# Optimization experiments

Hardware: AMD Instinct MI355X
Metric: run time of the kernel (lower is better)

## Reference

```python
import jax, jax.numpy as jnp
import numpy as np

B, L, H, NB, D, DH = 8, 4096, 16, 8, 1024, 128

def setup_inputs() -> dict:
    key = jax.random.key(0)
    ks = jax.random.split(key, 12)
    theta_path = jax.random.normal(ks[0], (B, L, H, NB), jnp.float32)
    content_emb = jax.random.normal(ks[1], (B, L, D), jnp.float32)
    s_in = 1.0 / np.sqrt(D).astype(np.float32)
    s_h = 1.0 / np.sqrt(DH).astype(np.float32)
    # log_R_head: Linear(D,128) -> GELU -> Linear(128, H*NB), last layer weight *0.01, bias 0
    r_w1 = jax.random.normal(ks[2], (D, DH), jnp.float32) * s_in
    r_b1 = jnp.zeros((DH,), jnp.float32)
    r_w2 = jax.random.normal(ks[3], (DH, H * NB), jnp.float32) * s_h * 0.01
    r_b2 = jnp.zeros((H * NB,), jnp.float32)
    # measure_head
    m_w1 = jax.random.normal(ks[4], (D, DH), jnp.float32) * s_in
    m_b1 = jax.random.normal(ks[5], (DH,), jnp.float32) * s_in
    m_w2 = jax.random.normal(ks[6], (DH, H * NB), jnp.float32) * s_h
    m_b2 = jax.random.normal(ks[7], (H * NB,), jnp.float32) * s_h
    log_Q = jnp.full((H, NB), -3.0, jnp.float32)
    log_R_avg = jnp.full((H, NB), 1.0, jnp.float32)
    return {"theta_path": theta_path, "content_emb": content_emb,
            "log_Q": log_Q, "log_R_avg": log_R_avg,
            "r_w1": r_w1, "r_b1": r_b1, "r_w2": r_w2, "r_b2": r_b2,
            "m_w1": m_w1, "m_b1": m_b1, "m_w2": m_w2, "m_b2": m_b2}

def _mlp(x, w1, b1, w2, b2):
    h = jax.nn.gelu(x @ w1 + b1, approximate=False)  # torch nn.GELU default = exact
    return h @ w2 + b2

def reference(theta_path, content_emb, log_Q, log_R_avg,
              r_w1, r_b1, r_w2, r_b2, m_w1, m_b1, m_w2, m_b2):
    b, l, h, nb = theta_path.shape
    log_R = jnp.clip(_mlp(content_emb, r_w1, r_b1, r_w2, r_b2).reshape(b, l, h, nb), -5.0, 5.0)
    R = jnp.exp(log_R)
    z = jnp.pi * jnp.tanh(_mlp(content_emb, m_w1, m_b1, m_w2, m_b2).reshape(b, l, h, nb))
    diff = z - theta_path
    nu = jnp.arctan2(jnp.sin(diff), jnp.cos(diff))  # wrap angle error to (-pi, pi]
    Q = jnp.exp(log_Q)
    Ravg = jnp.exp(log_R_avg)
    Pi_dare = 0.5 * (-Q + jnp.sqrt(Q * Q + 4.0 * Q * Ravg))  # [H, NB]
    Pi = jnp.broadcast_to(Pi_dare[None, None], (b, l, h, nb))
    K = Pi / jnp.maximum(Pi + R, 1e-8)
    alpha = 1.0 - K
    u = K * nu
    # affine associative scan over sequence dim: d_t = alpha_t * d_{t-1} + u_t
    def combine(c1, c2):
        a1, u1 = c1
        a2, u2 = c2
        return (a2 * a1, a2 * u1 + u2)
    _, d = jax.lax.associative_scan(combine, (alpha, u), axis=1)
    return (theta_path + d, Pi, K, R)
```

## Files before the change

### kernel.cpp

```cpp
#include <hip/hip_runtime.h>
#include <hip/hip_bf16.h>
#include <cstdint>
#include <cstddef>

#define TOK 32768
#define CCH 128
#define DIN 1024

typedef __attribute__((ext_vector_type(8))) short short8;
typedef __attribute__((ext_vector_type(4))) float f32x4;

#define LIST_CAP 262144u

static __device__ __forceinline__ uint16_t f2bf(float f) {
  __hip_bfloat16 h = __float2bfloat16(f);
  return __builtin_bit_cast(uint16_t, h);
}
static __device__ __forceinline__ float bf2f(uint16_t u) {
  __hip_bfloat16 h = __builtin_bit_cast(__hip_bfloat16, u);
  return __bfloat162float(h);
}
static __device__ __forceinline__ void splitbf(float x, uint16_t& hi, uint16_t& lo) {
  hi = f2bf(x);
  lo = f2bf(x - bf2f(hi));
}

__global__ void prep_kernel(const float* __restrict__ r_w1, const float* __restrict__ r_w2,
                            const float* __restrict__ m_w1, const float* __restrict__ m_w2,
                            const float* __restrict__ logQ, const float* __restrict__ logRavg,
                            uint16_t* __restrict__ W1r, uint16_t* __restrict__ W2r,
                            uint16_t* __restrict__ W1mh, uint16_t* __restrict__ W1ml,
                            uint16_t* __restrict__ W2mh, uint16_t* __restrict__ W2ml,
                            float* __restrict__ PiArr, unsigned int* __restrict__ cnt)
{
  int idx = blockIdx.x * 256 + threadIdx.x;
  if (idx == 0) cnt[0] = 0;
  if (idx < 131072) {
    int e = idx;
    int j = e & 7, lane = (e >> 3) & 63, nt = (e >> 9) & 7, c = (e >> 12) & 1, kt = e >> 13;
    int k = kt * 64 + c * 32 + (lane >> 4) * 8 + j;
    int n = nt * 16 + (lane & 15);
    W1r[e] = f2bf(r_w1[k * 128 + n]);
  } else if (idx < 147456) {
    int e = idx - 131072;
    int j = e & 7, l = (e >> 3) & 63, c = (e >> 9) & 3, t = e >> 11;
    int k = c * 32 + (l >> 4) * 8 + j;
    int col = t * 16 + (l & 15);
    W2r[e] = f2bf(r_w2[k * 128 + col]);
  } else if (idx < 278528) {
    int e = idx - 147456;
    int j = e & 7, lane = (e >> 3) & 63, nt = (e >> 9) & 7, c = (e >> 12) & 1, kt = e >> 13;
    int k = kt * 64 + c * 32 + (lane >> 4) * 8 + j;
    int n = nt * 16 + (lane & 15);
    uint16_t h, l;
    splitbf(m_w1[k * 128 + n], h, l);
    W1mh[e] = h; W1ml[e] = l;
  } else if (idx < 294912) {
    int e = idx - 278528;
    int j = e & 7, l = (e >> 3) & 63, c = (e >> 9) & 3, t = e >> 11;
    int k = c * 32 + (l >> 4) * 8 + j;
    int col = t * 16 + (l & 15);
    uint16_t h, lo;
    splitbf(m_w2[k * 128 + col], h, lo);
    W2mh[e] = h; W2ml[e] = lo;
  } else if (idx < 295040) {
    int i = idx - 294912;
    float Q = expf(logQ[i]);
    float Rv = expf(logRavg[i]);
    PiArr[i] = 0.5f * (-Q + sqrtf(Q * Q + 4.0f * Q * Rv));
  }
}

__global__ __launch_bounds__(512, 4) void fused_all(
    const float* __restrict__ X, const float* __restrict__ theta,
    const uint16_t* __restrict__ W1r, const uint16_t* __restrict__ W2r,
    const uint16_t* __restrict__ W1h, const uint16_t* __restrict__ W1l,
    const uint16_t* __restrict__ W2h, const uint16_t* __restrict__ W2l,
    const float* __restrict__ rB1, const float* __restrict__ rB2,
    const float* __restrict__ B1, const float* __restrict__ B2,
    const float* __restrict__ PiArr,
    float* __restrict__ out0, float* __restrict__ out1,
    float* __restrict__ out2, float* __restrict__ out3,
    float* __restrict__ AggA, float* __restrict__ AggU,
    unsigned int* __restrict__ cnt, unsigned int* __restrict__ list)
{
  union SM {
    struct { uint16_t Xh[2][64][64]; uint16_t Xl[2][64][64]; } s1;
    struct { uint16_t Hh[64][128]; uint16_t Hl[64][128]; uint16_t Hr[64][128]; } s2;
    struct { float2 Agg[4][4][128]; } s3;
  };
  __shared__ SM sm;

  const int tid = threadIdx.x;
  const int w = tid >> 6, lane = tid & 63;
  const int l15 = lane & 15, l4 = lane >> 4;
  const int tn = w;
  const int tok0 = blockIdx.x * 64;

  f32x4 accm[4], accr[4];
#pragma unroll
  for (int m = 0; m < 4; ++m) { accm[m] = 0.0f; accr[m] = 0.0f; }

  const int rr = tid >> 4, cc = tid & 15;
  const int wofs = (cc * 8) ^ ((rr & 7) << 4);
  float4 xa0, xa1;

  auto ldX = [&](int kt, float4& v0, float4& v1) {
    v0 = *reinterpret_cast<const float4*>(
        X + (size_t)(tok0 + rr) * DIN + kt * 64 + cc * 4);
    v1 = *reinterpret_cast<const float4*>(
        X + (size_t)(tok0 + rr + 32) * DIN + kt * 64 + cc * 4);
  };
  auto wrX = [&](int b, const float4& v0, const float4& v1) {
    ushort4 vh, vl;
    splitbf(v0.x, vh.x, vl.x);
    splitbf(v0.y, vh.y, vl.y);
    splitbf(v0.z, vh.z, vl.z);
    splitbf(v0.w, vh.w, vl.w);
    *reinterpret_cast<ushort4*>((char*)&sm.s1.Xh[b][rr][0] + wofs) = vh;
    *reinterpret_cast<ushort4*>((char*)&sm.s1.Xl[b][rr][0] + wofs) = vl;
    splitbf(v1.x, vh.x, vl.x);
    splitbf(v1.y, vh.y, vl.y);
    splitbf(v1.z, vh.z, vl.z);
    splitbf(v1.w, vh.w, vl.w);
    *reinterpret_cast<ushort4*>((char*)&sm.s1.Xh[b][rr + 32][0] + wofs) = vh;
    *reinterpret_cast<ushort4*>((char*)&sm.s1.Xl[b][rr + 32][0] + wofs) = vl;
  };
  auto ldB = [&](int kt, short8 (&h)[2], short8 (&l)[2], short8 (&r)[2]) {
#pragma unroll
    for (int c = 0; c < 2; ++c) {
      const size_t boff = (size_t)((((kt * 2 + c) * 8 + tn) * 64 + lane) * 8);
      h[c] = *reinterpret_cast<const short8*>(W1h + boff);
      l[c] = *reinterpret_cast<const short8*>(W1l + boff);
      r[c] = *reinterpret_cast<const short8*>(W1r + boff);
    }
  };

  short8 bhc[2], blc[2], brc[2], bhn[2], bln[2], brn[2];
  ldX(0, xa0, xa1);
  wrX(0, xa0, xa1);
  ldB(0, bhc, blc, brc);
  __syncthreads();

#pragma unroll
  for (int kt = 0; kt < 16; ++kt) {
    const int cur = kt & 1;

    if (kt < 15) {
      ldX(kt + 1, xa0, xa1);
      ldB(kt + 1, bhn, bln, brn);
    }

#pragma unroll
    for (int c = 0; c < 2; ++c) {
#pragma unroll
      for (int m = 0; m < 4; ++m) {
        const int row = m * 16 + l15;
        const int ob = (c * 64 + l4 * 16) ^ ((l15 & 7) << 4);
        const short8 ah = *reinterpret_cast<const short8*>((const char*)&sm.s1.Xh[cur][row][0] + ob);
        const short8 al = *reinterpret_cast<const short8*>((const char*)&sm.s1.Xl[cur][row][0] + ob);
        accm[m] = __builtin_amdgcn_mfma_f32_16x16x32_bf16(ah, bhc[c], accm[m], 0, 0, 0);
        accm[m] = __builtin_amdgcn_mfma_f32_16x16x32_bf16(al, bhc[c], accm[m], 0, 0, 0);
        accm[m] = __builtin_amdgcn_mfma_f32_16x16x32_bf16(ah, blc[c], accm[m], 0, 0, 0);
        accr[m] = __builtin_amdgcn_mfma_f32_16x16x32_bf16(ah, brc[c], accr[m], 0, 0, 0);
      }
    }

    if (kt < 15) wrX(cur ^ 1, xa0, xa1);
    __syncthreads();

#pragma unroll
    for (int c = 0; c < 2; ++c) { bhc[c] = bhn[c]; blc[c] = bln[c]; brc[c] = brn[c]; }
  }

  short8 b2h[4], b2l[4], b2r[4];
#pragma unroll
  for (int c2 = 0; c2 < 4; ++c2) {
    const size_t boff = (size_t)(((tn * 4 + c2) * 64 + lane) * 8);
    b2h[c2] = *reinterpret_cast<const short8*>(W2h + boff);
    b2l[c2] = *reinterpret_cast<const short8*>(W2l + boff);
    b2r[c2] = *reinterpret_cast<const short8*>(W2r + boff);
  }

  const int n = tn * 16 + l15;
  {
    const float b1m = B1[n];
    const float b1rr = rB1[n];
#pragma unroll
    for (int m = 0; m < 4; ++m)
#pragma unroll
      for (int r = 0; r < 4; ++r) {
        const int row = m * 16 + l4 * 4 + r;
        const int ob = (2 * n) ^ ((row & 7) << 4);
        const float v = accm[m][r] + b1m;
        const float ev = erff(v / 1.41421356237309515f);
        const float g = 0.5f * v * (ev + 1.0f);
        uint16_t gh, gl;
        splitbf(g, gh, gl);
        *reinterpret_cast<uint16_t*>((char*)&sm.s2.Hh[row][0] + ob) = gh;
        *reinterpret_cast<uint16_t*>((char*)&sm.s2.Hl[row][0] + ob) = gl;
        const float vr = accr[m][r] + b1rr;
        const float gr = 0.5f * vr * (1.0f + erff(vr * 0.70710678118654752f));
        *reinterpret_cast<uint16_t*>((char*)&sm.s2.Hr[row][0] + ob) = f2bf(gr);
      }
  }
  __syncthreads();

  f32x4 acc2m[4], acc2r[4];
#pragma unroll
  for (int m = 0; m < 4; ++m) { acc2m[m] = 0.0f; acc2r[m] = 0.0f; }

#pragma unroll
  for (int c2 = 0; c2 < 4; ++c2) {
#pragma unroll
    for (int m = 0; m < 4; ++m) {
      const int row = m * 16 + l15;
      const int ob = (c2 * 64 + l4 * 16) ^ ((l15 & 7) << 4);
      const short8 ah = *reinterpret_cast<const short8*>((const char*)&sm.s2.Hh[row][0] + ob);
      const short8 al = *reinterpret_cast<const short8*>((const char*)&sm.s2.Hl[row][0] + ob);
      const short8 ar = *reinterpret_cast<const short8*>((const char*)&sm.s2.Hr[row][0] + ob);
      acc2m[m] = __builtin_amdgcn_mfma_f32_16x16x32_bf16(ah, b2h[c2], acc2m[m], 0, 0, 0);
      acc2m[m] = __builtin_amdgcn_mfma_f32_16x16x32_bf16(al, b2h[c2], acc2m[m], 0, 0, 0);
      acc2m[m] = __builtin_amdgcn_mfma_f32_16x16x32_bf16(ah, b2l[c2], acc2m[m], 0, 0, 0);
      acc2r[m] = __builtin_amdgcn_mfma_f32_16x16x32_bf16(ar, b2r[c2], acc2r[m], 0, 0, 0);
    }
  }

  {
    const float b2 = rB2[n];
    const float piv = PiArr[n];
#pragma unroll
    for (int m = 0; m < 4; ++m)
#pragma unroll
      for (int r = 0; r < 4; ++r) {
        const int token = tok0 + m * 16 + l4 * 4 + r;
        float lr = acc2r[m][r] + b2;
        lr = fminf(fmaxf(lr, -5.0f), 5.0f);
        const float R = expf(lr);
        const float K = piv / fmaxf(piv + R, 1e-8f);
        const size_t off = (size_t)token * CCH + n;
        out1[off] = piv;
        out2[off] = K;
        out3[off] = R;
        acc2r[m][r] = K;
      }
  }

  {
    const float b2 = B2[n];
#pragma unroll
    for (int m = 0; m < 4; ++m)
#pragma unroll
      for (int r = 0; r < 4; ++r) {
        const int token = tok0 + m * 16 + l4 * 4 + r;
        const float mz = acc2m[m][r] + b2;
        const float z = 3.14159265358979323846f * tanhf(mz);
        const float d = z - theta[(size_t)token * CCH + n];
        const float wr = d - 6.2831853071795864769f * rintf(d * 0.15915494309189533577f);
        if (3.14159265358979323846f - fabsf(wr) < 3e-4f) {
          unsigned int p = atomicAdd(cnt, 1u);
          if (p < LIST_CAP) list[p] = (unsigned int)(token * CCH + n);
        }
        out0[(size_t)token * CCH + n] = wr;
        acc2m[m][r] = wr;
      }
  }

  __syncthreads();
#pragma unroll
  for (int m = 0; m < 4; ++m) {
    float A = 1.0f, U = 0.0f;
#pragma unroll
    for (int r = 0; r < 4; ++r) {
      const float k = acc2r[m][r];
      const float v = acc2m[m][r];
      const float a = 1.0f - k;
      A *= a;
      U = fmaf(a, U, k * v);
    }
    sm.s3.Agg[m][l4][n] = make_float2(A, U);
  }
  __syncthreads();
  if (tid < 128) {
    const int ch = tid;
    float A = 1.0f, U = 0.0f;
#pragma unroll
    for (int g = 0; g < 16; ++g) {
      const float2 au = sm.s3.Agg[g >> 2][g & 3][ch];
      U = fmaf(au.x, U, au.y);
      A *= au.x;
    }
    AggA[blockIdx.x * CCH + ch] = A;
    AggU[blockIdx.x * CCH + ch] = U;
  }
}

__global__ __launch_bounds__(128) void refine_nu(
    const float* __restrict__ X, const float* __restrict__ theta,
    const float* __restrict__ W1, const float* __restrict__ B1,
    const float* __restrict__ W2, const float* __restrict__ B2,
    const unsigned int* __restrict__ cnt, const unsigned int* __restrict__ list,
    float* __restrict__ out0)
{
  __shared__ float h[128];
  const int j = threadIdx.x;
  const unsigned int n = min(cnt[0], LIST_CAP);
  for (unsigned int e = blockIdx.x; e < n; e += gridDim.x) {
    const unsigned int idx = list[e];
    const int tok = (int)(idx >> 7), ch = (int)(idx & 127);
    const float* xr = X + (size_t)tok * DIN;
    float acc = 0.0f;
    for (int k = 0; k < DIN; ++k)
      acc = fmaf(xr[k], W1[(size_t)k * CCH + j], acc);
    const float v = acc + B1[j];
    const float ev = erff(v / 1.41421356237309515f);
    h[j] = 0.5f * v * (ev + 1.0f);
    __syncthreads();
    if (j == 0) {
      float a2 = 0.0f;
      for (int k = 0; k < CCH; ++k)
        a2 = fmaf(h[k], W2[(size_t)k * CCH + ch], a2);
      const float mz = a2 + B2[ch];
      const float z = 3.14159265358979323846f * tanhf(mz);
      const float d = z - theta[(size_t)tok * CCH + ch];
      out0[(size_t)tok * CCH + ch] = atan2f(sinf(d), cosf(d));
    }
    __syncthreads();
  }
}

__global__ __launch_bounds__(64) void refine_agg(
    const float* __restrict__ Kk, const float* __restrict__ nu,
    const unsigned int* __restrict__ cnt, const unsigned int* __restrict__ list,
    float* __restrict__ AggA, float* __restrict__ AggU)
{
  __shared__ float av[64], uv[64];
  const int i = threadIdx.x;
  const unsigned int n = min(cnt[0], LIST_CAP);
  for (unsigned int e = blockIdx.x; e < n; e += gridDim.x) {
    const unsigned int idx = list[e];
    const int ch = (int)(idx & 127);
    const int blk = (int)(idx >> 13);
    const size_t off = (size_t)(blk * 64 + i) * CCH + ch;
    const float k = Kk[off];
    const float v = nu[off];
    av[i] = 1.0f - k;
    uv[i] = k * v;
    __syncthreads();
    if (i == 0) {
      float A = 1.0f, U = 0.0f;
      for (int g = 0; g < 64; ++g) {
        U = fmaf(av[g], U, uv[g]);
        A *= av[g];
      }
      AggA[blk * CCH + ch] = A;
      AggU[blk * CCH + ch] = U;
    }
    __syncthreads();
  }
}

__global__ __launch_bounds__(256) void scan_pass2(
    const float* __restrict__ AggA, const float* __restrict__ AggU,
    float* __restrict__ Carry)
{
  const int wid = blockIdx.x * 4 + (threadIdx.x >> 6);
  const int b = wid >> 7, ch = wid & 127;
  const int g = threadIdx.x & 63;
  const size_t idx = (size_t)(b * 64 + g) * CCH + ch;
  float A = AggA[idx];
  float U = AggU[idx];
#pragma unroll
  for (int s = 1; s < 64; s <<= 1) {
    const float pA = __shfl_up(A, s);
    const float pU = __shfl_up(U, s);
    if (g >= s) {
      U = fmaf(A, pU, U);
      A = A * pA;
    }
  }
  float cU = __shfl_up(U, 1);
  if (g == 0) cU = 0.0f;
  Carry[idx] = cU;
}

__global__ __launch_bounds__(128) void scan_pass3(
    const float* __restrict__ Kk, const float* __restrict__ theta,
    const float* __restrict__ Carry, float* __restrict__ out0)
{
  __shared__ float kb[64 * CCH];
  __shared__ float vb[64 * CCH];
  const int c = threadIdx.x;
  const int blk = blockIdx.x;
  const size_t base = (size_t)blk * 64 * CCH;
#pragma unroll
  for (int i = 0; i < 16; ++i) {
    const int e = i * 128 + c;
    reinterpret_cast<float4*>(kb)[e] = reinterpret_cast<const float4*>(Kk + base)[e];
    reinterpret_cast<float4*>(vb)[e] = reinterpret_cast<const float4*>(out0 + base)[e];
  }
  __syncthreads();
  float d = Carry[blk * CCH + c];
#pragma unroll 8
  for (int i = 0; i < 64; ++i) {
    const float k = kb[i * CCH + c];
    const float v = vb[i * CCH + c];
    d = fmaf(1.0f - k, d, k * v);
    const size_t off = base + (size_t)i * CCH + c;
    out0[off] = theta[off] + d;
  }
}

extern "C" void kernel_launch(void* const* d_in, const int* in_sizes, int n_in,
                              void* d_out, int out_size, void* d_ws, size_t ws_size,
                              hipStream_t stream) {
  const float* theta   = (const float*)d_in[0];
  const float* X       = (const float*)d_in[1];
  const float* logQ    = (const float*)d_in[2];
  const float* logRavg = (const float*)d_in[3];
  const float* r_w1    = (const float*)d_in[4];
  const float* r_b1    = (const float*)d_in[5];
  const float* r_w2    = (const float*)d_in[6];
  const float* r_b2    = (const float*)d_in[7];
  const float* m_w1    = (const float*)d_in[8];
  const float* m_b1    = (const float*)d_in[9];
  const float* m_w2    = (const float*)d_in[10];
  const float* m_b2    = (const float*)d_in[11];

  float* out0 = (float*)d_out;
  float* out1 = out0 + 4194304;
  float* out2 = out0 + 2 * 4194304;
  float* out3 = out0 + 3 * 4194304;

  char* ws = (char*)d_ws;
  uint16_t* W1r  = (uint16_t*)(ws);
  uint16_t* W2r  = (uint16_t*)(ws + 262144);
  float* PiArr   = (float*)(ws + 295936);
  float* AggA    = (float*)(ws + 296448);
  float* AggU    = (float*)(ws + 558592);
  float* Carry   = (float*)(ws + 820736);
  unsigned int* cnt  = (unsigned int*)(ws + 1082880);
  unsigned int* list = (unsigned int*)(ws + 1083136);
  uint16_t* W1mh = (uint16_t*)(ws + 2131712);
  uint16_t* W1ml = (uint16_t*)(ws + 2393856);
  uint16_t* W2mh = (uint16_t*)(ws + 2656000);
  uint16_t* W2ml = (uint16_t*)(ws + 2688768);

  prep_kernel<<<1153, 256, 0, stream>>>(r_w1, r_w2, m_w1, m_w2, logQ, logRavg,
                                        W1r, W2r, W1mh, W1ml, W2mh, W2ml,
                                        PiArr, cnt);
  fused_all<<<512, 512, 0, stream>>>(X, theta, W1r, W2r, W1mh, W1ml, W2mh, W2ml,
                                     r_b1, r_b2, m_b1, m_b2, PiArr,
                                     out0, out1, out2, out3, AggA, AggU, cnt, list);
  refine_nu<<<1024, 128, 0, stream>>>(X, theta, m_w1, m_b1, m_w2, m_b2,
                                      cnt, list, out0);
  refine_agg<<<1024, 64, 0, stream>>>(out2, out0, cnt, list, AggA, AggU);
  scan_pass2<<<256, 256, 0, stream>>>(AggA, AggU, Carry);
  scan_pass3<<<512, 128, 0, stream>>>(out2, theta, Carry, out0);
}
```

Baseline: 123.4 us.

## Process two K-tiles per barrier with a four-stage X shared buffer

The first GEMM loop over the 1024-wide input is restructured to handle two 64-wide K tiles per iteration, with four X buffers in shared memory. That halves the number of __syncthreads barriers and issues two global X loads ahead per iteration. In exchange it uses more registers for the extra prefetched tiles, and the enlarged stage-1 union member raises LDS per block. The W1 fragment load for the second tile is now issued inside the same iteration that consumes it, so that load is less hidden.

```diff
diff --git a/kernel.cpp b/kernel.cpp
--- a/kernel.cpp
+++ b/kernel.cpp
@@ -85,7 +85,7 @@
     unsigned int* __restrict__ cnt, unsigned int* __restrict__ list)
 {
   union SM {
-    struct { uint16_t Xh[2][64][64]; uint16_t Xl[2][64][64]; } s1;
+    struct { uint16_t Xh[4][64][64]; uint16_t Xl[4][64][64]; } s1;
     struct { uint16_t Hh[64][128]; uint16_t Hl[64][128]; uint16_t Hr[64][128]; } s2;
     struct { float2 Agg[4][4][128]; } s3;
   };
@@ -103,7 +103,7 @@
 
   const int rr = tid >> 4, cc = tid & 15;
   const int wofs = (cc * 8) ^ ((rr & 7) << 4);
-  float4 xa0, xa1;
+  float4 xa0, xa1, xb0, xb1;
 
   auto ldX = [&](int kt, float4& v0, float4& v1) {
     v0 = *reinterpret_cast<const float4*>(
@@ -135,42 +135,49 @@
       r[c] = *reinterpret_cast<const short8*>(W1r + boff);
     }
   };
-
-  short8 bhc[2], blc[2], brc[2], bhn[2], bln[2], brn[2];
-  ldX(0, xa0, xa1);
-  wrX(0, xa0, xa1);
-  ldB(0, bhc, blc, brc);
-  __syncthreads();
-
-#pragma unroll
-  for (int kt = 0; kt < 16; ++kt) {
-    const int cur = kt & 1;
-
-    if (kt < 15) {
-      ldX(kt + 1, xa0, xa1);
-      ldB(kt + 1, bhn, bln, brn);
-    }
-
+  auto cluster = [&](int buf, short8 (&bh)[2], short8 (&bl)[2], short8 (&br)[2]) {
 #pragma unroll
     for (int c = 0; c < 2; ++c) {
 #pragma unroll
       for (int m = 0; m < 4; ++m) {
         const int row = m * 16 + l15;
         const int ob = (c * 64 + l4 * 16) ^ ((l15 & 7) << 4);
-        const short8 ah = *reinterpret_cast<const short8*>((const char*)&sm.s1.Xh[cur][row][0] + ob);
-        const short8 al = *reinterpret_cast<const short8*>((const char*)&sm.s1.Xl[cur][row][0] + ob);
-        accm[m] = __builtin_amdgcn_mfma_f32_16x16x32_bf16(ah, bhc[c], accm[m], 0, 0, 0);
-        accm[m] = __builtin_amdgcn_mfma_f32_16x16x32_bf16(al, bhc[c], accm[m], 0, 0, 0);
-        accm[m] = __builtin_amdgcn_mfma_f32_16x16x32_bf16(ah, blc[c], accm[m], 0, 0, 0);
-        accr[m] = __builtin_amdgcn_mfma_f32_16x16x32_bf16(ah, brc[c], accr[m], 0, 0, 0);
+        const short8 ah = *reinterpret_cast<const short8*>((const char*)&sm.s1.Xh[buf][row][0] + ob);
+        const short8 al = *reinterpret_cast<const short8*>((const char*)&sm.s1.Xl[buf][row][0] + ob);
+        accm[m] = __builtin_amdgcn_mfma_f32_16x16x32_bf16(ah, bh[c], accm[m], 0, 0, 0);
+        accm[m] = __builtin_amdgcn_mfma_f32_16x16x32_bf16(al, bh[c], accm[m], 0, 0, 0);
+        accm[m] = __builtin_amdgcn_mfma_f32_16x16x32_bf16(ah, bl[c], accm[m], 0, 0, 0);
+        accr[m] = __builtin_amdgcn_mfma_f32_16x16x32_bf16(ah, br[c], accr[m], 0, 0, 0);
       }
     }
-
-    if (kt < 15) wrX(cur ^ 1, xa0, xa1);
+  };
+
+  short8 bch[2], bcl[2], bcr[2], bnh[2], bnl[2], bnr[2];
+  ldX(0, xa0, xa1);
+  wrX(0, xa0, xa1);
+  ldX(1, xa0, xa1);
+  wrX(1, xa0, xa1);
+  ldB(0, bch, bcl, bcr);
+  __syncthreads();
+
+#pragma unroll
+  for (int i = 0; i < 8; ++i) {
+    const int kt0 = 2 * i, kt1 = 2 * i + 1;
+    if (i < 7) {
+      ldX(kt0 + 2, xa0, xa1);
+      ldX(kt1 + 2, xb0, xb1);
+    }
+    ldB(kt1, bnh, bnl, bnr);
+
+    cluster(kt0 & 3, bch, bcl, bcr);
+    cluster(kt1 & 3, bnh, bnl, bnr);
+
+    if (i < 7) {
+      wrX((kt0 + 2) & 3, xa0, xa1);
+      wrX((kt1 + 2) & 3, xb0, xb1);
+      ldB(kt0 + 2, bch, bcl, bcr);
+    }
     __syncthreads();
-
-#pragma unroll
-    for (int c = 0; c < 2; ++c) { bhc[c] = bhn[c]; blc[c] = bln[c]; brc[c] = brn[c]; }
   }
 
   short8 b2h[4], b2l[4], b2r[4];
```

Result: slower. 131.1 us (+6.3%).

## Retile fused MLP kernel to 2x2 warp grid with split-phase weight prefetch

Applied to the files above, without the earlier changes.

Each of the 8 waves now computes a 32-token by 32-channel tile in a 2x2 (tm,tn) arrangement instead of 64 tokens by 16 channels. Every B-fragment register load and every shared-memory A fragment now feeds two MFMAs, which cuts per-wave LDS reads of the X and H tiles. The first-layer weight prefetch is split into half-step chunks, loaded between the two MFMA clusters, and second-layer weights are double-buffered per k-chunk, which lowers peak register use. The cost is more global weight loads per wave and a changed register and scheduling profile.

```diff
diff --git a/kernel.cpp b/kernel.cpp
--- a/kernel.cpp
+++ b/kernel.cpp
@@ -94,12 +94,14 @@
   const int tid = threadIdx.x;
   const int w = tid >> 6, lane = tid & 63;
   const int l15 = lane & 15, l4 = lane >> 4;
-  const int tn = w;
+  const int tm = w >> 2, tn = w & 3;
   const int tok0 = blockIdx.x * 64;
 
-  f32x4 accm[4], accr[4];
-#pragma unroll
-  for (int m = 0; m < 4; ++m) { accm[m] = 0.0f; accr[m] = 0.0f; }
+  f32x4 accm[2][2], accr[2][2];
+#pragma unroll
+  for (int mm = 0; mm < 2; ++mm)
+#pragma unroll
+    for (int t = 0; t < 2; ++t) { accm[mm][t] = 0.0f; accr[mm][t] = 0.0f; }
 
   const int rr = tid >> 4, cc = tid & 15;
   const int wofs = (cc * 8) ^ ((rr & 7) << 4);
@@ -126,115 +128,129 @@
     *reinterpret_cast<ushort4*>((char*)&sm.s1.Xh[b][rr + 32][0] + wofs) = vh;
     *reinterpret_cast<ushort4*>((char*)&sm.s1.Xl[b][rr + 32][0] + wofs) = vl;
   };
-  auto ldB = [&](int kt, short8 (&h)[2], short8 (&l)[2], short8 (&r)[2]) {
-#pragma unroll
-    for (int c = 0; c < 2; ++c) {
-      const size_t boff = (size_t)((((kt * 2 + c) * 8 + tn) * 64 + lane) * 8);
-      h[c] = *reinterpret_cast<const short8*>(W1h + boff);
-      l[c] = *reinterpret_cast<const short8*>(W1l + boff);
-      r[c] = *reinterpret_cast<const short8*>(W1r + boff);
+  auto ldB = [&](int kt, int c, short8 (&h)[2], short8 (&l)[2], short8 (&r)[2]) {
+#pragma unroll
+    for (int t = 0; t < 2; ++t) {
+      const size_t boff = (size_t)((((kt * 2 + c) * 8 + (tn * 2 + t)) * 64 + lane) * 8);
+      h[t] = *reinterpret_cast<const short8*>(W1h + boff);
+      l[t] = *reinterpret_cast<const short8*>(W1l + boff);
+      r[t] = *reinterpret_cast<const short8*>(W1r + boff);
     }
   };
-
-  short8 bhc[2], blc[2], brc[2], bhn[2], bln[2], brn[2];
+  auto cluster = [&](int buf, int c, short8 (&bh)[2], short8 (&bl)[2], short8 (&br)[2]) {
+#pragma unroll
+    for (int mm = 0; mm < 2; ++mm) {
+      const int row = (tm * 2 + mm) * 16 + l15;
+      const int ob = (c * 64 + l4 * 16) ^ ((l15 & 7) << 4);
+      const short8 ah = *reinterpret_cast<const short8*>((const char*)&sm.s1.Xh[buf][row][0] + ob);
+      const short8 al = *reinterpret_cast<const short8*>((const char*)&sm.s1.Xl[buf][row][0] + ob);
+#pragma unroll
+      for (int t = 0; t < 2; ++t) {
+        accm[mm][t] = __builtin_amdgcn_mfma_f32_16x16x32_bf16(ah, bh[t], accm[mm][t], 0, 0, 0);
+        accm[mm][t] = __builtin_amdgcn_mfma_f32_16x16x32_bf16(al, bh[t], accm[mm][t], 0, 0, 0);
+        accm[mm][t] = __builtin_amdgcn_mfma_f32_16x16x32_bf16(ah, bl[t], accm[mm][t], 0, 0, 0);
+        accr[mm][t] = __builtin_amdgcn_mfma_f32_16x16x32_bf16(ah, br[t], accr[mm][t], 0, 0, 0);
+      }
+    }
+  };
+
+  short8 b0h[2], b0l[2], b0r[2], b1h[2], b1l[2], b1r[2];
   ldX(0, xa0, xa1);
   wrX(0, xa0, xa1);
-  ldB(0, bhc, blc, brc);
+  ldB(0, 0, b0h, b0l, b0r);
   __syncthreads();
 
 #pragma unroll
   for (int kt = 0; kt < 16; ++kt) {
     const int cur = kt & 1;
-
-    if (kt < 15) {
-      ldX(kt + 1, xa0, xa1);
-      ldB(kt + 1, bhn, bln, brn);
-    }
-
-#pragma unroll
-    for (int c = 0; c < 2; ++c) {
-#pragma unroll
-      for (int m = 0; m < 4; ++m) {
-        const int row = m * 16 + l15;
-        const int ob = (c * 64 + l4 * 16) ^ ((l15 & 7) << 4);
-        const short8 ah = *reinterpret_cast<const short8*>((const char*)&sm.s1.Xh[cur][row][0] + ob);
-        const short8 al = *reinterpret_cast<const short8*>((const char*)&sm.s1.Xl[cur][row][0] + ob);
-        accm[m] = __builtin_amdgcn_mfma_f32_16x16x32_bf16(ah, bhc[c], accm[m], 0, 0, 0);
-        accm[m] = __builtin_amdgcn_mfma_f32_16x16x32_bf16(al, bhc[c], accm[m], 0, 0, 0);
-        accm[m] = __builtin_amdgcn_mfma_f32_16x16x32_bf16(ah, blc[c], accm[m], 0, 0, 0);
-        accr[m] = __builtin_amdgcn_mfma_f32_16x16x32_bf16(ah, brc[c], accr[m], 0, 0, 0);
-      }
-    }
-
+    if (kt < 15) ldX(kt + 1, xa0, xa1);
+    ldB(kt, 1, b1h, b1l, b1r);
+    cluster(cur, 0, b0h, b0l, b0r);
+    if (kt < 15) ldB(kt + 1, 0, b0h, b0l, b0r);
+    cluster(cur, 1, b1h, b1l, b1r);
     if (kt < 15) wrX(cur ^ 1, xa0, xa1);
     __syncthreads();
-
-#pragma unroll
-    for (int c = 0; c < 2; ++c) { bhc[c] = bhn[c]; blc[c] = bln[c]; brc[c] = brn[c]; }
-  }
-
-  short8 b2h[4], b2l[4], b2r[4];
-#pragma unroll
-  for (int c2 = 0; c2 < 4; ++c2) {
-    const size_t boff = (size_t)(((tn * 4 + c2) * 64 + lane) * 8);
-    b2h[c2] = *reinterpret_cast<const short8*>(W2h + boff);
-    b2l[c2] = *reinterpret_cast<const short8*>(W2l + boff);
-    b2r[c2] = *reinterpret_cast<const short8*>(W2r + boff);
-  }
-
-  const int n = tn * 16 + l15;
-  {
+  }
+
+#pragma unroll
+  for (int t = 0; t < 2; ++t) {
+    const int n = (tn * 2 + t) * 16 + l15;
     const float b1m = B1[n];
     const float b1rr = rB1[n];
 #pragma unroll
-    for (int m = 0; m < 4; ++m)
+    for (int mm = 0; mm < 2; ++mm)
 #pragma unroll
       for (int r = 0; r < 4; ++r) {
-        const int row = m * 16 + l4 * 4 + r;
+        const int row = (tm * 2 + mm) * 16 + l4 * 4 + r;
         const int ob = (2 * n) ^ ((row & 7) << 4);
-        const float v = accm[m][r] + b1m;
+        const float v = accm[mm][t][r] + b1m;
         const float ev = erff(v / 1.41421356237309515f);
         const float g = 0.5f * v * (ev + 1.0f);
         uint16_t gh, gl;
         splitbf(g, gh, gl);
         *reinterpret_cast<uint16_t*>((char*)&sm.s2.Hh[row][0] + ob) = gh;
         *reinterpret_cast<uint16_t*>((char*)&sm.s2.Hl[row][0] + ob) = gl;
-        const float vr = accr[m][r] + b1rr;
+        const float vr = accr[mm][t][r] + b1rr;
         const float gr = 0.5f * vr * (1.0f + erff(vr * 0.70710678118654752f));
         *reinterpret_cast<uint16_t*>((char*)&sm.s2.Hr[row][0] + ob) = f2bf(gr);
       }
   }
   __syncthreads();
 
-  f32x4 acc2m[4], acc2r[4];
-#pragma unroll
-  for (int m = 0; m < 4; ++m) { acc2m[m] = 0.0f; acc2r[m] = 0.0f; }
-
+  f32x4 acc2m[2][2], acc2r[2][2];
+#pragma unroll
+  for (int mm = 0; mm < 2; ++mm)
+#pragma unroll
+    for (int t = 0; t < 2; ++t) { acc2m[mm][t] = 0.0f; acc2r[mm][t] = 0.0f; }
+
+  short8 w2h[2][2], w2l[2][2], w2r[2][2];
+#pragma unroll
+  for (int t = 0; t < 2; ++t) {
+    const size_t boff = (size_t)((((tn * 2 + t) * 4 + 0) * 64 + lane) * 8);
+    w2h[0][t] = *reinterpret_cast<const short8*>(W2h + boff);
+    w2l[0][t] = *reinterpret_cast<const short8*>(W2l + boff);
+    w2r[0][t] = *reinterpret_cast<const short8*>(W2r + boff);
+  }
 #pragma unroll
   for (int c2 = 0; c2 < 4; ++c2) {
-#pragma unroll
-    for (int m = 0; m < 4; ++m) {
-      const int row = m * 16 + l15;
+    const int cb = c2 & 1;
+    if (c2 < 3) {
+#pragma unroll
+      for (int t = 0; t < 2; ++t) {
+        const size_t boff = (size_t)((((tn * 2 + t) * 4 + (c2 + 1)) * 64 + lane) * 8);
+        w2h[cb ^ 1][t] = *reinterpret_cast<const short8*>(W2h + boff);
+        w2l[cb ^ 1][t] = *reinterpret_cast<const short8*>(W2l + boff);
+        w2r[cb ^ 1][t] = *reinterpret_cast<const short8*>(W2r + boff);
+      }
+    }
+#pragma unroll
+    for (int mm = 0; mm < 2; ++mm) {
+      const int row = (tm * 2 + mm) * 16 + l15;
       const int ob = (c2 * 64 + l4 * 16) ^ ((l15 & 7) << 4);
       const short8 ah = *reinterpret_cast<const short8*>((const char*)&sm.s2.Hh[row][0] + ob);
       const short8 al = *reinterpret_cast<const short8*>((const char*)&sm.s2.Hl[row][0] + ob);
       const short8 ar = *reinterpret_cast<const short8*>((const char*)&sm.s2.Hr[row][0] + ob);
-      acc2m[m] = __builtin_amdgcn_mfma_f32_16x16x32_bf16(ah, b2h[c2], acc2m[m], 0, 0, 0);
-      acc2m[m] = __builtin_amdgcn_mfma_f32_16x16x32_bf16(al, b2h[c2], acc2m[m], 0, 0, 0);
-      acc2m[m] = __builtin_amdgcn_mfma_f32_16x16x32_bf16(ah, b2l[c2], acc2m[m], 0, 0, 0);
-      acc2r[m] = __builtin_amdgcn_mfma_f32_16x16x32_bf16(ar, b2r[c2], acc2r[m], 0, 0, 0);
-    }
-  }
-
-  {
+#pragma unroll
+      for (int t = 0; t < 2; ++t) {
+        acc2m[mm][t] = __builtin_amdgcn_mfma_f32_16x16x32_bf16(ah, w2h[cb][t], acc2m[mm][t], 0, 0, 0);
+        acc2m[mm][t] = __builtin_amdgcn_mfma_f32_16x16x32_bf16(al, w2h[cb][t], acc2m[mm][t], 0, 0, 0);
+        acc2m[mm][t] = __builtin_amdgcn_mfma_f32_16x16x32_bf16(ah, w2l[cb][t], acc2m[mm][t], 0, 0, 0);
+        acc2r[mm][t] = __builtin_amdgcn_mfma_f32_16x16x32_bf16(ar, w2r[cb][t], acc2r[mm][t], 0, 0, 0);
+      }
+    }
+  }
+
+#pragma unroll
+  for (int t = 0; t < 2; ++t) {
+    const int n = (tn * 2 + t) * 16 + l15;
     const float b2 = rB2[n];
     const float piv = PiArr[n];
 #pragma unroll
-    for (int m = 0; m < 4; ++m)
+    for (int mm = 0; mm < 2; ++mm)
 #pragma unroll
       for (int r = 0; r < 4; ++r) {
-        const int token = tok0 + m * 16 + l4 * 4 + r;
-        float lr = acc2r[m][r] + b2;
+        const int token = tok0 + (tm * 2 + mm) * 16 + l4 * 4 + r;
+        float lr = acc2r[mm][t][r] + b2;
         lr = fminf(fmaxf(lr, -5.0f), 5.0f);
         const float R = expf(lr);
         const float K = piv / fmaxf(piv + R, 1e-8f);
@@ -242,18 +258,20 @@
         out1[off] = piv;
         out2[off] = K;
         out3[off] = R;
-        acc2r[m][r] = K;
-      }
-  }
-
-  {
+        acc2r[mm][t][r] = K;
+      }
+  }
+
+#pragma unroll
+  for (int t = 0; t < 2; ++t) {
+    const int n = (tn * 2 + t) * 16 + l15;
     const float b2 = B2[n];
 #pragma unroll
-    for (int m = 0; m < 4; ++m)
+    for (int mm = 0; mm < 2; ++mm)
 #pragma unroll
       for (int r = 0; r < 4; ++r) {
-        const int token = tok0 + m * 16 + l4 * 4 + r;
-        const float mz = acc2m[m][r] + b2;
+        const int token = tok0 + (tm * 2 + mm) * 16 + l4 * 4 + r;
+        const float mz = acc2m[mm][t][r] + b2;
         const float z = 3.14159265358979323846f * tanhf(mz);
         const float d = z - theta[(size_t)token * CCH + n];
         const float wr = d - 6.2831853071795864769f * rintf(d * 0.15915494309189533577f);
@@ -262,23 +280,27 @@
           if (p < LIST_CAP) list[p] = (unsigned int)(token * CCH + n);
         }
         out0[(size_t)token * CCH + n] = wr;
-        acc2m[m][r] = wr;
+        acc2m[mm][t][r] = wr;
       }
   }
 
   __syncthreads();
 #pragma unroll
-  for (int m = 0; m < 4; ++m) {
-    float A = 1.0f, U = 0.0f;
-#pragma unroll
-    for (int r = 0; r < 4; ++r) {
-      const float k = acc2r[m][r];
-      const float v = acc2m[m][r];
-      const float a = 1.0f - k;
-      A *= a;
-      U = fmaf(a, U, k * v);
-    }
-    sm.s3.Agg[m][l4][n] = make_float2(A, U);
+  for (int t = 0; t < 2; ++t) {
+    const int n = (tn * 2 + t) * 16 + l15;
+#pragma unroll
+    for (int mm = 0; mm < 2; ++mm) {
+      float A = 1.0f, U = 0.0f;
+#pragma unroll
+      for (int r = 0; r < 4; ++r) {
+        const float k = acc2r[mm][t][r];
+        const float v = acc2m[mm][t][r];
+        const float a = 1.0f - k;
+        A *= a;
+        U = fmaf(a, U, k * v);
+      }
+      sm.s3.Agg[tm * 2 + mm][l4][n] = make_float2(A, U);
+    }
   }
   __syncthreads();
   if (tid < 128) {
```

Result: no change. 121.9 us, median of 2 (-1.2%).
